# Optimization experiments

Measured on AMD Instinct MI355X. Metric: run time of the kernel, lower is better.

Reference implementation:

```python
import jax, jax.numpy as jnp
import numpy as np

B, T, C, HEADS = 4, 2305, 384, 6
BN_EPS = 1e-5


def setup_inputs() -> dict:
    key = jax.random.key(0)
    ks = jax.random.split(key, 24)
    d = {
        'x': jax.random.normal(ks[0], (B, T, C), dtype=jnp.float32),
        'h': 48,
        'w': 48,
        # depthwise conv kernels (groups=C, no bias): OIHW with I=1
        'kq': jax.random.normal(ks[1], (C, 1, 3, 3), dtype=jnp.float32) * 0.1,
        'kk': jax.random.normal(ks[2], (C, 1, 3, 3), dtype=jnp.float32) * 0.1,
        'kv': jax.random.normal(ks[3], (C, 1, 3, 3), dtype=jnp.float32) * 0.1,
        # BatchNorm (eval mode) params per projection: gamma, beta, running_mean, running_var
        'gq': jax.random.normal(ks[4], (C,), dtype=jnp.float32) * 0.1 + 1.0,
        'bq': jax.random.normal(ks[5], (C,), dtype=jnp.float32) * 0.1,
        'mq': jax.random.normal(ks[6], (C,), dtype=jnp.float32) * 0.1,
        'vq': jax.random.uniform(ks[7], (C,), dtype=jnp.float32) + 0.5,
        'gk': jax.random.normal(ks[8], (C,), dtype=jnp.float32) * 0.1 + 1.0,
        'bk': jax.random.normal(ks[9], (C,), dtype=jnp.float32) * 0.1,
        'mk': jax.random.normal(ks[10], (C,), dtype=jnp.float32) * 0.1,
        'vk': jax.random.uniform(ks[11], (C,), dtype=jnp.float32) + 0.5,
        'gv': jax.random.normal(ks[12], (C,), dtype=jnp.float32) * 0.1 + 1.0,
        'bv': jax.random.normal(ks[13], (C,), dtype=jnp.float32) * 0.1,
        'mv': jax.random.normal(ks[14], (C,), dtype=jnp.float32) * 0.1,
        'vv': jax.random.uniform(ks[15], (C,), dtype=jnp.float32) + 0.5,
        # Linear weights, torch convention [out, in]; qkv_bias=False
        'Wq': jax.random.normal(ks[16], (C, C), dtype=jnp.float32) / np.sqrt(C),
        'Wk': jax.random.normal(ks[17], (C, C), dtype=jnp.float32) / np.sqrt(C),
        'Wv': jax.random.normal(ks[18], (C, C), dtype=jnp.float32) / np.sqrt(C),
        'Wo': jax.random.normal(ks[19], (C, C), dtype=jnp.float32) / np.sqrt(C),
        'bo': jax.random.normal(ks[20], (C,), dtype=jnp.float32) * 0.01,
    }
    return d


def _dw_bn(xi, kern, gamma, beta, mean, var, h, w):
    # xi: [B, C, h, w]; depthwise 3x3 conv, stride 1, pad 1, then eval-mode BN
    y = jax.lax.conv_general_dilated(
        xi, kern, window_strides=(1, 1), padding=((1, 1), (1, 1)),
        feature_group_count=C, dimension_numbers=('NCHW', 'OIHW', 'NCHW'))
    scale = (gamma / jnp.sqrt(var + BN_EPS))[None, :, None, None]
    y = (y - mean[None, :, None, None]) * scale + beta[None, :, None, None]
    # b c h w -> b (h w) c
    return y.transpose(0, 2, 3, 1).reshape(y.shape[0], h * w, C)


def _forward(x, kq, kk, kv, gq, bq, mq, vq, gk, bk, mk, vk, gv, bv, mv, vv,
             Wq, Wk, Wv, Wo, bo, h, w):
    b, t, c = x.shape
    scale = c ** (-0.5)  # note: dim**-0.5, NOT head_dim**-0.5 (as in source)
    cls_tok, xs = x[:, :1], x[:, 1:]
    xi = xs.reshape(b, h, w, c).transpose(0, 3, 1, 2)  # b (h w) c -> b c h w
    q = jnp.concatenate([cls_tok, _dw_bn(xi, kq, gq, bq, mq, vq, h, w)], axis=1)
    k = jnp.concatenate([cls_tok, _dw_bn(xi, kk, gk, bk, mk, vk, h, w)], axis=1)
    v = jnp.concatenate([cls_tok, _dw_bn(xi, kv, gv, bv, mv, vv, h, w)], axis=1)
    dh = c // HEADS
    q = (q @ Wq.T).reshape(b, t, HEADS, dh).transpose(0, 2, 1, 3)  # bhtd
    k = (k @ Wk.T).reshape(b, t, HEADS, dh).transpose(0, 2, 1, 3)
    v = (v @ Wv.T).reshape(b, t, HEADS, dh).transpose(0, 2, 1, 3)
    attn = jax.nn.softmax(jnp.einsum('bhld,bhtd->bhlt', q, k) * scale, axis=-1)
    out = jnp.einsum('bhlt,bhtd->bhld', attn, v)
    out = out.transpose(0, 2, 1, 3).reshape(b, t, c)
    return out @ Wo.T + bo


def reference(x, kq, kk, kv, gq, bq, mq, vq, gk, bk, mk, vk, gv, bv, mv, vv,
              Wq, Wk, Wv, Wo, bo, h, w):
    return _forward(x, kq, kk, kv, gq, bq, mq, vq, gk, bk, mk, vk, gv, bv,
                    mv, vv, Wq, Wk, Wv, Wo, bo, h, w)
```

## Files before the change

### kernel.cpp

```cpp
#include <hip/hip_runtime.h>
#include <hip/hip_bf16.h>

#define BN 4
#define TT 2305
#define CC 384
#define HH 6
#define DH 64
#define GW 48
#define BH (BN*HH)
#define TP 2368
#define TQP 2560
#define MF 9220
#define MP 9344
#define MB2 73
#define NSPL 2
#define C2 0.07362223f

typedef __hip_bfloat16 bf16;
typedef __attribute__((ext_vector_type(8))) short short8;
typedef __attribute__((ext_vector_type(4))) float floatx4;
typedef __attribute__((ext_vector_type(16))) float floatx16;

#define MFMA16(a,b,c) __builtin_amdgcn_mfma_f32_16x16x32_bf16((a),(b),(c),0,0,0)
#define MFMA32(a,b,c) __builtin_amdgcn_mfma_f32_32x32x16_bf16((a),(b),(c),0,0,0)

__device__ __forceinline__ unsigned pack2(float a, float b) {
    bf16 lo = __float2bfloat16(a);
    bf16 hi = __float2bfloat16(b);
    unsigned short ul = *reinterpret_cast<unsigned short*>(&lo);
    unsigned short uh = *reinterpret_cast<unsigned short*>(&hi);
    return (unsigned)ul | ((unsigned)uh << 16);
}
__device__ __forceinline__ float bu2f(unsigned u16) {
    unsigned v = u16 << 16;
    return *reinterpret_cast<float*>(&v);
}

__global__ __launch_bounds__(384)
void conv_bn(const float* __restrict__ x,
             const float* __restrict__ kq, const float* __restrict__ kk, const float* __restrict__ kv,
             const float* __restrict__ gq, const float* __restrict__ bq, const float* __restrict__ mq, const float* __restrict__ vq,
             const float* __restrict__ gk, const float* __restrict__ bk, const float* __restrict__ mk, const float* __restrict__ vk,
             const float* __restrict__ gv, const float* __restrict__ bv, const float* __restrict__ mv, const float* __restrict__ vv,
             const float* __restrict__ Wq, const float* __restrict__ Wk,
             const float* __restrict__ Wv, const float* __restrict__ Wo,
             bf16* __restrict__ wqb, bf16* __restrict__ wkb,
             bf16* __restrict__ wvb, bf16* __restrict__ wob,
             bf16* __restrict__ cq, bf16* __restrict__ ck, bf16* __restrict__ cv)
{
    {
        const int i = blockIdx.x * 384 + threadIdx.x;
        if (i < CC * CC) {
            wqb[i] = __float2bfloat16(Wq[i]);
            wkb[i] = __float2bfloat16(Wk[i]);
            wvb[i] = __float2bfloat16(Wv[i]);
            wob[i] = __float2bfloat16(Wo[i]);
        }
    }

    const int n = blockIdx.x;
    const int b = n / 289;
    const int t0 = (n % 289) * 8;
    const int c = threadIdx.x;
    const size_t xbase = (size_t)b * TT * CC;

    const float sq = gq[c] * rsqrtf(vq[c] + 1e-5f), oq = bq[c] - mq[c] * sq;
    const float sk = gk[c] * rsqrtf(vk[c] + 1e-5f), ok = bk[c] - mk[c] * sk;
    const float sv = gv[c] * rsqrtf(vv[c] + 1e-5f), ov = bv[c] - mv[c] * sv;
    float wq9[9], wk9[9], wv9[9];
    #pragma unroll
    for (int u = 0; u < 9; u++) {
        wq9[u] = kq[c * 9 + u]; wk9[u] = kk[c * 9 + u]; wv9[u] = kv[c * 9 + u];
    }

    for (int g = 0; g < 8; g++) {
        const int t = t0 + g;
        if (t >= TT) break;
        const size_t mrow = (size_t)(b * TT + t) * CC + c;
        if (t == 0) {
            bf16 xv = __float2bfloat16(x[xbase + c]);
            cq[mrow] = xv; ck[mrow] = xv; cv[mrow] = xv;
        } else {
            const int s = t - 1, i = s / GW, j = s % GW;
            float aq = 0.f, ak = 0.f, av = 0.f;
            #pragma unroll
            for (int di = 0; di < 3; di++) {
                int ii = i + di - 1;
                if (ii < 0 || ii >= GW) continue;
                #pragma unroll
                for (int dj = 0; dj < 3; dj++) {
                    int jj = j + dj - 1;
                    if (jj < 0 || jj >= GW) continue;
                    float xv = x[xbase + (size_t)(1 + ii * GW + jj) * CC + c];
                    int u = di * 3 + dj;
                    aq += xv * wq9[u]; ak += xv * wk9[u]; av += xv * wv9[u];
                }
            }
            cq[mrow] = __float2bfloat16(aq * sq + oq);
            ck[mrow] = __float2bfloat16(ak * sk + ok);
            cv[mrow] = __float2bfloat16(av * sv + ov);
        }
    }
}

__global__ __launch_bounds__(256)
void qkv_gemm(const bf16* __restrict__ cq, const bf16* __restrict__ ck, const bf16* __restrict__ cv,
              const bf16* __restrict__ Wq, const bf16* __restrict__ Wk, const bf16* __restrict__ Wv,
              bf16* __restrict__ q, bf16* __restrict__ k, bf16* __restrict__ vT)
{
    const int bt = blockIdx.x;
    const int b = bt / 10;
    const int m0 = (bt % 10) * 256;
    const int n0 = blockIdx.y * 64;
    const int w = threadIdx.x >> 6, lane = threadIdx.x & 63;
    const int lm = lane & 15, q4 = lane >> 4;
    const int which = n0 / CC;
    const int obase = n0 % CC;
    const bf16* A = (which == 0) ? cq : (which == 1) ? ck : cv;
    const bf16* W = (which == 0) ? Wq : (which == 1) ? Wk : Wv;

    __shared__ __align__(16) bf16 TR[64 * 264];

    size_t arow[4];
    #pragma unroll
    for (int st = 0; st < 4; st++) {
        int t = m0 + st * 64 + w * 16 + lm;
        if (t >= TT) t = TT - 1;
        arow[st] = (size_t)(b * TT + t) * CC;
    }

    floatx4 acc[4][4];
    #pragma unroll
    for (int st = 0; st < 4; st++)
        #pragma unroll
        for (int n = 0; n < 4; n++) acc[st][n] = (floatx4){0.f, 0.f, 0.f, 0.f};

    #pragma unroll 2
    for (int kc = 0; kc < CC / 32; kc++) {
        short8 a[4];
        #pragma unroll
        for (int st = 0; st < 4; st++)
            a[st] = *(const short8*)(A + arow[st] + kc * 32 + q4 * 8);
        #pragma unroll
        for (int n = 0; n < 4; n++) {
            short8 bfr = *(const short8*)(W + (size_t)(obase + n * 16 + lm) * CC + kc * 32 + q4 * 8);
            #pragma unroll
            for (int st = 0; st < 4; st++)
                acc[st][n] = MFMA16(a[st], bfr, acc[st][n]);
        }
    }

    if (which == 2) {
        #pragma unroll
        for (int st = 0; st < 4; st++)
            #pragma unroll
            for (int n = 0; n < 4; n++) {
                const int ol = n * 16 + lm;
                const int ml = st * 64 + w * 16 + q4 * 4;
                uint2 pkd = { pack2(acc[st][n][0], acc[st][n][1]),
                              pack2(acc[st][n][2], acc[st][n][3]) };
                *(uint2*)&TR[ol * 264 + ml] = pkd;
            }
        __syncthreads();
        const int h = obase >> 6;
        const int o = threadIdx.x >> 2;
        const int seg = threadIdx.x & 3;
        const size_t vrow = ((size_t)(b * HH + h) * DH + o) * TP;
        #pragma unroll
        for (int j = 0; j < 8; j++) {
            const int ml = seg * 64 + j * 8;
            const int t = m0 + ml;
            uint4 val = *(const uint4*)&TR[o * 264 + ml];
            if (t + 8 <= TT) {
                *(uint4*)(vT + vrow + t) = val;
            } else if (t < TT) {
                const bf16* pv = (const bf16*)&val;
                for (int e = 0; e < 8 && t + e < TT; e++) vT[vrow + t + e] = pv[e];
            }
        }
    } else {
        #pragma unroll
        for (int st = 0; st < 4; st++)
            #pragma unroll
            for (int n = 0; n < 4; n++) {
                const int o = obase + n * 16 + lm;
                const int h = o >> 6, d = o & 63;
                #pragma unroll
                for (int r = 0; r < 4; r++) {
                    const int t = m0 + st * 64 + w * 16 + q4 * 4 + r;
                    if (t >= TT) continue;
                    bf16 val = __float2bfloat16(acc[st][n][r]);
                    if (which == 0)
                        q[((size_t)(b * HH + h) * TQP + t) * DH + d] = val;
                    else
                        k[((size_t)(b * HH + h) * TP + t) * DH + d] = val;
                }
            }
    }
}

__global__ __launch_bounds__(256, 2)
void flash(const bf16* __restrict__ q, const bf16* __restrict__ k,
           const bf16* __restrict__ vT, bf16* __restrict__ OP, float* __restrict__ ML)
{
    const int id = blockIdx.x;
    const int bh = id % BH;
    const int rest = id / BH;
    const int z = rest % NSPL;
    const int qt = rest / NSPL;
    const int tid = threadIdx.x;
    const int w = tid >> 6, lane = tid & 63;
    const int q31 = lane & 31, hh = lane >> 5;
    const int q0 = qt * 256 + w * 64;
    const size_t kbase = (size_t)bh * TP * DH;
    const size_t qbase = (size_t)bh * TQP * DH;

    __shared__ __align__(16) bf16 Ks[2][64 * 64];
    __shared__ __align__(16) bf16 Vs[2][64 * 64];

    short8 qf[2][4];
    #pragma unroll
    for (int s = 0; s < 2; s++) {
        const bf16* qrow = q + qbase + (size_t)(q0 + s * 32 + q31) * DH;
        #pragma unroll
        for (int kc = 0; kc < 4; kc++)
            qf[s][kc] = *(const short8*)(qrow + kc * 16 + hh * 8);
    }

    floatx16 of[2][2];
    #pragma unroll
    for (int s = 0; s < 2; s++)
        #pragma unroll
        for (int dt = 0; dt < 2; dt++)
            #pragma unroll
            for (int r = 0; r < 16; r++) of[s][dt][r] = 0.f;
    float m2[2] = {-1e30f, -1e30f}, lsum[2] = {0.f, 0.f};

    const int tstart = z ? 19 : 0;
    const int tend   = z ? 37 : 19;

    const int tr0 = tid >> 3,          c80 = tid & 7;
    const int tr1 = (tid + 256) >> 3,  c81 = tid & 7;
    const int so0 = tr0 * 64 + ((c80 ^ (tr0 & 7)) * 8);
    const int so1 = tr1 * 64 + ((c81 ^ (tr1 & 7)) * 8);

    uint4 kreg[2], vreg[2];
    {
        const int t0 = tstart * 64;
        kreg[0] = *(const uint4*)(k + kbase + (size_t)(t0 + tr0) * DH + c80 * 8);
        vreg[0] = *(const uint4*)(vT + kbase + (size_t)tr0 * TP + t0 + c80 * 8);
        kreg[1] = *(const uint4*)(k + kbase + (size_t)(t0 + tr1) * DH + c81 * 8);
        vreg[1] = *(const uint4*)(vT + kbase + (size_t)tr1 * TP + t0 + c81 * 8);
    }
    *(uint4*)&Ks[0][so0] = kreg[0];
    *(uint4*)&Vs[0][so0] = vreg[0];
    *(uint4*)&Ks[0][so1] = kreg[1];
    *(uint4*)&Vs[0][so1] = vreg[1];

    for (int tc = tstart; tc < tend; tc++) {
        const int cur = (tc - tstart) & 1;
        const int t0 = tc * 64;
        __syncthreads();
        const bool more = (tc + 1 < tend);
        if (more) {
            const int t1 = t0 + 64;
            kreg[0] = *(const uint4*)(k + kbase + (size_t)(t1 + tr0) * DH + c80 * 8);
            vreg[0] = *(const uint4*)(vT + kbase + (size_t)tr0 * TP + t1 + c80 * 8);
            kreg[1] = *(const uint4*)(k + kbase + (size_t)(t1 + tr1) * DH + c81 * 8);
            vreg[1] = *(const uint4*)(vT + kbase + (size_t)tr1 * TP + t1 + c81 * 8);
        }
        const bf16* Kc = Ks[cur];
        const bf16* Vc = Vs[cur];

        short8 ka[2][4], va[2][4];
        #pragma unroll
        for (int mt = 0; mt < 2; mt++)
            #pragma unroll
            for (int kc = 0; kc < 4; kc++) {
                const int row = mt * 32 + q31, c = 2 * kc + hh;
                ka[mt][kc] = *(const short8*)&Kc[row * 64 + ((c ^ (row & 7)) * 8)];
                va[mt][kc] = *(const short8*)&Vc[row * 64 + ((c ^ (row & 7)) * 8)];
            }
        const bool tail = (t0 + 64 > TT);

        #pragma unroll
        for (int s = 0; s < 2; s++) {
            floatx16 sv[2];
            #pragma unroll
            for (int mt = 0; mt < 2; mt++)
                #pragma unroll
                for (int r = 0; r < 16; r++) sv[mt][r] = 0.f;
            #pragma unroll
            for (int kc = 0; kc < 4; kc++) {
                sv[0] = MFMA32(ka[0][kc], qf[s][kc], sv[0]);
                sv[1] = MFMA32(ka[1][kc], qf[s][kc], sv[1]);
            }
            if (tail) {
                #pragma unroll
                for (int mt = 0; mt < 2; mt++)
                    #pragma unroll
                    for (int r = 0; r < 16; r++) {
                        const int tl = t0 + mt * 32 + (r & 3) + 8 * (r >> 2) + 4 * hh;
                        if (tl >= TT) sv[mt][r] = -1e30f;
                    }
            }
            float rm = sv[0][0];
            #pragma unroll
            for (int r = 1; r < 16; r++) rm = fmaxf(rm, sv[0][r]);
            #pragma unroll
            for (int r = 0; r < 16; r++) rm = fmaxf(rm, sv[1][r]);
            rm = fmaxf(rm, __shfl_xor(rm, 32));
            const float mn = fmaxf(m2[s], rm * C2);
            const float alpha = __builtin_amdgcn_exp2f(m2[s] - mn);
            m2[s] = mn;
            const float negm = -mn;
            float rs = 0.f;
            unsigned pk[2][8];
            #pragma unroll
            for (int mt = 0; mt < 2; mt++)
                #pragma unroll
                for (int p = 0; p < 8; p++) {
                    const float p0 = __builtin_amdgcn_exp2f(fmaf(sv[mt][2 * p], C2, negm));
                    const float p1 = __builtin_amdgcn_exp2f(fmaf(sv[mt][2 * p + 1], C2, negm));
                    rs += p0 + p1;
                    pk[mt][p] = pack2(p0, p1);
                }
            rs += __shfl_xor(rs, 32);
            lsum[s] = lsum[s] * alpha + rs;
            #pragma unroll
            for (int dt = 0; dt < 2; dt++)
                #pragma unroll
                for (int r = 0; r < 16; r++) of[s][dt][r] *= alpha;

            #pragma unroll
            for (int kc = 0; kc < 4; kc++) {
                const int u0 = 2 * kc, u1 = 2 * kc + 1;
                const unsigned P0a = pk[u0 >> 2][2 * (u0 & 3)];
                const unsigned P0b = pk[u0 >> 2][2 * (u0 & 3) + 1];
                const unsigned P1a = pk[u1 >> 2][2 * (u1 & 3)];
                const unsigned P1b = pk[u1 >> 2][2 * (u1 & 3) + 1];
                const unsigned X1 = hh ? P0a : P1a;
                const unsigned X2 = hh ? P0b : P1b;
                const unsigned Y1 = __shfl_xor(X1, 32);
                const unsigned Y2 = __shfl_xor(X2, 32);
                unsigned dw[4];
                dw[0] = hh ? Y1 : P0a;
                dw[1] = hh ? Y2 : P0b;
                dw[2] = hh ? P1a : Y1;
                dw[3] = hh ? P1b : Y2;
                short8 pb = *reinterpret_cast<short8*>(dw);
                of[s][0] = MFMA32(va[0][kc], pb, of[s][0]);
                of[s][1] = MFMA32(va[1][kc], pb, of[s][1]);
            }
        }

        if (more) {
            bf16* Kn = Ks[1 - cur];
            bf16* Vn = Vs[1 - cur];
            *(uint4*)&Kn[so0] = kreg[0];
            *(uint4*)&Vn[so0] = vreg[0];
            *(uint4*)&Kn[so1] = kreg[1];
            *(uint4*)&Vn[so1] = vreg[1];
        }
    }

    #pragma unroll
    for (int s = 0; s < 2; s++) {
        const int qrow = q0 + s * 32 + q31;
        if (qrow >= TT) continue;
        bf16* orow = OP + ((size_t)(z * BH + bh) * TT + qrow) * DH;
        #pragma unroll
        for (int dt = 0; dt < 2; dt++)
            #pragma unroll
            for (int p = 0; p < 4; p++) {
                const int d = dt * 32 + 8 * p + 4 * hh;
                unsigned lo = pack2(of[s][dt][4 * p], of[s][dt][4 * p + 1]);
                unsigned hi = pack2(of[s][dt][4 * p + 2], of[s][dt][4 * p + 3]);
                uint2 st = {lo, hi};
                *(uint2*)(orow + d) = st;
            }
        if (hh == 0) {
            float2 ml = {m2[s], lsum[s]};
            *(float2*)&ML[((size_t)(z * BH + bh) * TT + qrow) * 2] = ml;
        }
    }
}

__global__ __launch_bounds__(256)
void merge(const bf16* __restrict__ OP, const float* __restrict__ ML,
           bf16* __restrict__ att)
{
    const int idx = blockIdx.x * 256 + threadIdx.x;
    if (idx >= BH * TT * 16) return;
    const int quad = idx & 15;
    const int pair = idx >> 4;
    const int bh = pair / TT, row = pair % TT;
    const int b = bh / HH, h = bh % HH;
    const int d0 = quad * 4;

    float2 ml[NSPL];
    #pragma unroll
    for (int z = 0; z < NSPL; z++)
        ml[z] = *(const float2*)&ML[((size_t)(z * BH + bh) * TT + row) * 2];
    float M = ml[0].x;
    #pragma unroll
    for (int z = 1; z < NSPL; z++) M = fmaxf(M, ml[z].x);
    float wz[NSPL], den = 0.f;
    #pragma unroll
    for (int z = 0; z < NSPL; z++) {
        wz[z] = __builtin_amdgcn_exp2f(ml[z].x - M);
        den += ml[z].y * wz[z];
    }
    const float inv = 1.f / den;

    float o0 = 0.f, o1 = 0.f, o2 = 0.f, o3 = 0.f;
    #pragma unroll
    for (int z = 0; z < NSPL; z++) {
        const float s = wz[z] * inv;
        const uint2 a = *(const uint2*)&OP[((size_t)(z * BH + bh) * TT + row) * DH + d0];
        o0 += bu2f(a.x & 0xffffu) * s;
        o1 += bu2f(a.x >> 16)     * s;
        o2 += bu2f(a.y & 0xffffu) * s;
        o3 += bu2f(a.y >> 16)     * s;
    }
    uint2 st = {pack2(o0, o1), pack2(o2, o3)};
    *(uint2*)&att[((size_t)(b * TT + row) * CC) + h * DH + d0] = st;
}

__global__ __launch_bounds__(256)
void out_gemm(const bf16* __restrict__ att, const bf16* __restrict__ Wo_bf,
              const float* __restrict__ bo, float* __restrict__ out)
{
    const int m0 = blockIdx.x * 128;
    const int n0 = blockIdx.y * 64;
    const int w = threadIdx.x >> 6, lane = threadIdx.x & 63;
    const int lm = lane & 15, q4 = lane >> 4;

    const size_t ar0 = (size_t)(m0 + w * 16 + lm) * CC;
    floatx4 acc[2][4];
    #pragma unroll
    for (int st = 0; st < 2; st++)
        #pragma unroll
        for (int n = 0; n < 4; n++) acc[st][n] = (floatx4){0.f, 0.f, 0.f, 0.f};

    #pragma unroll 4
    for (int kc = 0; kc < CC / 32; kc++) {
        short8 a0 = *(const short8*)(att + ar0 + kc * 32 + q4 * 8);
        short8 a1 = *(const short8*)(att + ar0 + (size_t)64 * CC + kc * 32 + q4 * 8);
        #pragma unroll
        for (int n = 0; n < 4; n++) {
            short8 bfr = *(const short8*)(Wo_bf + (size_t)(n0 + n * 16 + lm) * CC + kc * 32 + q4 * 8);
            acc[0][n] = MFMA16(a0, bfr, acc[0][n]);
            acc[1][n] = MFMA16(a1, bfr, acc[1][n]);
        }
    }

    #pragma unroll
    for (int st = 0; st < 2; st++)
        #pragma unroll
        for (int n = 0; n < 4; n++) {
            const int o = n0 + n * 16 + lm;
            const float bias = bo[o];
            #pragma unroll
            for (int r = 0; r < 4; r++) {
                const int m = m0 + st * 64 + w * 16 + q4 * 4 + r;
                if (m < MF) out[(size_t)m * CC + o] = acc[st][n][r] + bias;
            }
        }
}

extern "C" void kernel_launch(void* const* d_in, const int* in_sizes, int n_in,
                              void* d_out, int out_size, void* d_ws, size_t ws_size,
                              hipStream_t stream)
{
    const float* x  = (const float*)d_in[0];
    const float* kq = (const float*)d_in[3];
    const float* kk = (const float*)d_in[4];
    const float* kv = (const float*)d_in[5];
    const float* gq = (const float*)d_in[6];
    const float* bq = (const float*)d_in[7];
    const float* mq = (const float*)d_in[8];
    const float* vq = (const float*)d_in[9];
    const float* gk = (const float*)d_in[10];
    const float* bk = (const float*)d_in[11];
    const float* mk = (const float*)d_in[12];
    const float* vk = (const float*)d_in[13];
    const float* gv = (const float*)d_in[14];
    const float* bv = (const float*)d_in[15];
    const float* mv = (const float*)d_in[16];
    const float* vv = (const float*)d_in[17];
    const float* Wq = (const float*)d_in[18];
    const float* Wk = (const float*)d_in[19];
    const float* Wv = (const float*)d_in[20];
    const float* Wo = (const float*)d_in[21];
    const float* bo = (const float*)d_in[22];

    char* ws = (char*)d_ws;
    const size_t SZ_CONV = (size_t)MP * CC * 2;
    const size_t SZ_Q    = (size_t)BH * TQP * DH * 2;
    const size_t SZ_K    = (size_t)BH * TP * DH * 2;
    const size_t SZ_W    = (size_t)CC * CC * 2;
    size_t off = 0;
    bf16* cq   = (bf16*)(ws + off); off += SZ_CONV;
    bf16* ck   = (bf16*)(ws + off); off += SZ_CONV;
    bf16* cv   = (bf16*)(ws + off); off += SZ_CONV;
    bf16* qb   = (bf16*)(ws + off); off += SZ_Q;
    bf16* kb   = (bf16*)(ws + off); off += SZ_K;
    bf16* vTb  = (bf16*)(ws + off); off += SZ_K;
    bf16* attb = (bf16*)(ws + off); off += SZ_CONV;
    bf16* wqb  = (bf16*)(ws + off); off += SZ_W;
    bf16* wkb  = (bf16*)(ws + off); off += SZ_W;
    bf16* wvb  = (bf16*)(ws + off); off += SZ_W;
    bf16* wob  = (bf16*)(ws + off); off += SZ_W;
    bf16*  OP = (bf16*)ws;
    float* ML = (float*)(ws + off); off += (size_t)NSPL * BH * TT * 2 * 4;

    conv_bn<<<BN * 289, 384, 0, stream>>>(x, kq, kk, kv,
                                          gq, bq, mq, vq,
                                          gk, bk, mk, vk,
                                          gv, bv, mv, vv,
                                          Wq, Wk, Wv, Wo,
                                          wqb, wkb, wvb, wob,
                                          cq, ck, cv);
    qkv_gemm<<<dim3(40, 18), 256, 0, stream>>>(cq, ck, cv, wqb, wkb, wvb, qb, kb, vTb);
    flash<<<10 * NSPL * BH, 256, 0, stream>>>(qb, kb, vTb, OP, ML);
    merge<<<(BH * TT * 16 + 255) / 256, 256, 0, stream>>>(OP, ML, attb);
    out_gemm<<<dim3(MB2, 6), 256, 0, stream>>>(attb, wob, bo, (float*)d_out);
}
```

Measured before the change: 287.3 us.

## Load K/V fragments directly from global memory instead of LDS double buffering

The flash attention kernel stops staging K and V^T tiles in shared memory with register prefetch and double buffering. Each wave now reads its MFMA operands straight from global memory, which removes the barriers and LDS traffic. The cost is that every wave in the block reads the same K/V data separately, relying on the cache, and global load latency is no longer hidden by a prefetch.

New measurement: 283.1 us. Within noise of the previous version (-1.5%).

```diff
diff --git a/kernel.cpp b/kernel.cpp
--- a/kernel.cpp
+++ b/kernel.cpp
@@ -215,9 +215,6 @@
     const size_t kbase = (size_t)bh * TP * DH;
     const size_t qbase = (size_t)bh * TQP * DH;
 
-    __shared__ __align__(16) bf16 Ks[2][64 * 64];
-    __shared__ __align__(16) bf16 Vs[2][64 * 64];
-
     short8 qf[2][4];
     #pragma unroll
     for (int s = 0; s < 2; s++) {
@@ -239,38 +236,10 @@
     const int tstart = z ? 19 : 0;
     const int tend   = z ? 37 : 19;
 
-    const int tr0 = tid >> 3,          c80 = tid & 7;
-    const int tr1 = (tid + 256) >> 3,  c81 = tid & 7;
-    const int so0 = tr0 * 64 + ((c80 ^ (tr0 & 7)) * 8);
-    const int so1 = tr1 * 64 + ((c81 ^ (tr1 & 7)) * 8);
-
-    uint4 kreg[2], vreg[2];
-    {
-        const int t0 = tstart * 64;
-        kreg[0] = *(const uint4*)(k + kbase + (size_t)(t0 + tr0) * DH + c80 * 8);
-        vreg[0] = *(const uint4*)(vT + kbase + (size_t)tr0 * TP + t0 + c80 * 8);
-        kreg[1] = *(const uint4*)(k + kbase + (size_t)(t0 + tr1) * DH + c81 * 8);
-        vreg[1] = *(const uint4*)(vT + kbase + (size_t)tr1 * TP + t0 + c81 * 8);
-    }
-    *(uint4*)&Ks[0][so0] = kreg[0];
-    *(uint4*)&Vs[0][so0] = vreg[0];
-    *(uint4*)&Ks[0][so1] = kreg[1];
-    *(uint4*)&Vs[0][so1] = vreg[1];
-
     for (int tc = tstart; tc < tend; tc++) {
-        const int cur = (tc - tstart) & 1;
         const int t0 = tc * 64;
-        __syncthreads();
-        const bool more = (tc + 1 < tend);
-        if (more) {
-            const int t1 = t0 + 64;
-            kreg[0] = *(const uint4*)(k + kbase + (size_t)(t1 + tr0) * DH + c80 * 8);
-            vreg[0] = *(const uint4*)(vT + kbase + (size_t)tr0 * TP + t1 + c80 * 8);
-            kreg[1] = *(const uint4*)(k + kbase + (size_t)(t1 + tr1) * DH + c81 * 8);
-            vreg[1] = *(const uint4*)(vT + kbase + (size_t)tr1 * TP + t1 + c81 * 8);
-        }
-        const bf16* Kc = Ks[cur];
-        const bf16* Vc = Vs[cur];
+        const bf16* kt = k + kbase + (size_t)t0 * DH;
+        const bf16* vt = vT + kbase + t0;
 
         short8 ka[2][4], va[2][4];
         #pragma unroll
@@ -278,8 +247,8 @@
             #pragma unroll
             for (int kc = 0; kc < 4; kc++) {
                 const int row = mt * 32 + q31, c = 2 * kc + hh;
-                ka[mt][kc] = *(const short8*)&Kc[row * 64 + ((c ^ (row & 7)) * 8)];
-                va[mt][kc] = *(const short8*)&Vc[row * 64 + ((c ^ (row & 7)) * 8)];
+                ka[mt][kc] = *(const short8*)(kt + (size_t)row * DH + c * 8);
+                va[mt][kc] = *(const short8*)(vt + (size_t)row * TP + c * 8);
             }
         const bool tail = (t0 + 64 > TT);
 
@@ -352,15 +321,6 @@
                 of[s][0] = MFMA32(va[0][kc], pb, of[s][0]);
                 of[s][1] = MFMA32(va[1][kc], pb, of[s][1]);
             }
-        }
-
-        if (more) {
-            bf16* Kn = Ks[1 - cur];
-            bf16* Vn = Vs[1 - cur];
-            *(uint4*)&Kn[so0] = kreg[0];
-            *(uint4*)&Vn[so0] = vreg[0];
-            *(uint4*)&Kn[so1] = kreg[1];
-            *(uint4*)&Vn[so1] = vreg[1];
         }
     }
 
```
